# Kernel tuning notes

Measured on AMD Instinct MI355X. Metric: run time of the kernel, lower is better.

## Reference

```python
import jax, jax.numpy as jnp
import numpy as np

SIGMA = 4.0
RADIUS = int(4.0 * SIGMA + 0.5)  # scipy gaussian_filter truncate=4.0 -> radius 16


def _gaussian_kernel():
    x = jnp.arange(-RADIUS, RADIUS + 1, dtype=jnp.float32)
    k = jnp.exp(-0.5 * (x / SIGMA) ** 2)
    return k / k.sum()


def _blur_last_axis(x):
    # separable 1D gaussian along last axis with reflect padding (scipy default mode)
    k = _gaussian_kernel()
    pad = [(0, 0)] * (x.ndim - 1) + [(RADIUS, RADIUS)]
    xp = jnp.pad(x, pad, mode='reflect')
    xr = xp.reshape(-1, 1, xp.shape[-1])  # [N, C=1, L]
    out = jax.lax.conv_general_dilated(xr, k.reshape(1, 1, -1), (1,), 'VALID')
    return out.reshape(x.shape)


def _gaussian_blur2d(img):
    # img: [B, H, W]
    img = _blur_last_axis(img)                       # blur W
    img = jnp.swapaxes(_blur_last_axis(jnp.swapaxes(img, -1, -2)), -1, -2)  # blur H
    return img


def setup_inputs() -> dict:
    key = jax.random.key(0)
    k1, k2 = jax.random.split(key)
    M, Q, D = 50000, 3136, 1024
    return {
        'coreset': jax.random.normal(k1, (M, D), dtype=jnp.float32),
        'features': jax.random.normal(k2, (Q, D), dtype=jnp.float32),
        'batchsize': 4,
        'grid_h': 28,
        'grid_w': 28,
        'out_h': 224,
        'out_w': 224,
    }


def reference(coreset, features, batchsize, grid_h, grid_w, out_h, out_w):
    # _compute_batchwise_differences: sqrt(clamp(|a|^2 - 2ab + |b|^2, 0))
    a2 = jnp.sum(coreset * coreset, axis=-1, keepdims=True)      # [M, 1]
    b2 = jnp.sum(features * features, axis=-1)[None, :]           # [1, Q]
    ab = jnp.einsum('md,qd->mq', coreset, features)               # [M, Q]
    dists = jnp.sqrt(jnp.clip(a2 - 2.0 * ab + b2, 0.0, None))     # [M, Q]
    patch_scores = dists.min(axis=0)                              # [Q] = min(0).values

    # unpatch_scores + PatchMaker.score (max over patches)
    per_image = patch_scores.reshape(batchsize, -1)               # [B, P]
    image_scores = per_image.max(axis=-1)                         # [B]

    # RescaleSegmentor.convert_to_segmentation: bilinear upsample + gaussian blur
    grid = patch_scores.reshape(batchsize, grid_h, grid_w)        # [B, Hp, Wp]
    masks = jax.image.resize(grid, (batchsize, out_h, out_w), method='bilinear')
    masks = _gaussian_blur2d(masks)                               # sigma=4 smoothing
    return image_scores, masks
```

## Files before the change

kernel.cpp:

```cpp
#include <hip/hip_runtime.h>


typedef unsigned short ushort_t;
typedef unsigned int uint32;
typedef __bf16 bf16x8 __attribute__((ext_vector_type(8)));
typedef float f32x4 __attribute__((ext_vector_type(4)));

#define M_ROWS 50000
#define M_PAD  50176
#define M_TILES 196
#define Q_ROWS 3136
#define Q_PAD  3328
#define Q_TILES 13
#define DDIM   1024
#define NKT    16
#define FLT_BIG 3.402823466e+38f

typedef __attribute__((address_space(1))) const void* as1_cvoid;
typedef __attribute__((address_space(3))) void* as3_void;

__device__ __forceinline__ void load16_lds(const void* g, void* l) {
  __builtin_amdgcn_global_load_lds((as1_cvoid)g, (as3_void)l, 16, 0, 0);
}

__device__ __forceinline__ ushort_t f2bf(float f) {
  uint32 u = __float_as_uint(f);
  u += 0x7FFFu + ((u >> 16) & 1u);
  return (ushort_t)(u >> 16);
}
__device__ __forceinline__ uint32 f2key(float f) {
  uint32 b = __float_as_uint(f);
  return (b & 0x80000000u) ? ~b : (b | 0x80000000u);
}
__device__ __forceinline__ float key2f(uint32 k) {
  uint32 b = (k & 0x80000000u) ? (k ^ 0x80000000u) : ~k;
  return __uint_as_float(b);
}

#define WAITVM6 asm volatile("s_waitcnt vmcnt(6)" ::: "memory")
#define WAITVM0 asm volatile("s_waitcnt vmcnt(0)" ::: "memory")
#define WAITVM8 asm volatile("s_waitcnt vmcnt(8)" ::: "memory")
#define LGKM0   asm volatile("s_waitcnt lgkmcnt(0)" ::: "memory")
#define BAR()   __builtin_amdgcn_s_barrier()

__global__ void k_init(uint32* __restrict__ mk) {
  int i = blockIdx.x * 256 + threadIdx.x;
  if (i < Q_PAD) mk[i] = 0xFFFFFFFFu;
}

__global__ void k_convert(const float* __restrict__ src, ushort_t* __restrict__ dst,
                          float* __restrict__ norm, int valid_rows, float pad_norm) {
  const int row = blockIdx.x * 4 + (threadIdx.x >> 6);
  const int lane = threadIdx.x & 63;
  if (row < valid_rows) {
    const float4* s = (const float4*)(src + (size_t)row * DDIM);
    ushort4* d = (ushort4*)(dst + (size_t)row * DDIM);
    float ss = 0.f;
    #pragma unroll
    for (int u = 0; u < 4; ++u) {
      const float4 v = s[lane + 64 * u];
      ss += v.x * v.x + v.y * v.y + v.z * v.z + v.w * v.w;
      ushort4 o;
      o.x = f2bf(v.x); o.y = f2bf(v.y); o.z = f2bf(v.z); o.w = f2bf(v.w);
      d[lane + 64 * u] = o;
    }
    #pragma unroll
    for (int off = 32; off; off >>= 1) ss += __shfl_xor(ss, off);
    if (lane == 0) norm[row] = ss;
  } else {
    ushort4 z; z.x = z.y = z.z = z.w = 0;
    ushort4* d = (ushort4*)(dst + (size_t)row * DDIM);
    #pragma unroll
    for (int u = 0; u < 4; ++u) d[lane + 64 * u] = z;
    if (lane == 0) norm[row] = pad_norm;
  }
}

__global__ __launch_bounds__(512, 2) void k_gemm_min(
    const ushort_t* __restrict__ A,
    const ushort_t* __restrict__ B,
    const float* __restrict__ a2, const float* __restrict__ b2,
    uint32* __restrict__ mk) {
  __shared__ __align__(16) ushort_t As[2][256 * 64];
  __shared__ __align__(16) ushort_t Bs[2][256 * 64];
  __shared__ float a2s[256];
  __shared__ float red[4][64];

  const int tid = threadIdx.x;
  const int lane = tid & 63;
  const int wid = tid >> 6;
  const int wr = wid >> 2;
  const int wc = wid & 3;

  const int nwg = M_TILES * Q_TILES;
  const int q8 = nwg >> 3, r8 = nwg & 7;
  const int w = blockIdx.x;
  const int xcd = w & 7, idx = w >> 3;
  const int nw = (xcd < r8 ? xcd * (q8 + 1) : r8 * (q8 + 1) + (xcd - r8) * q8) + idx;
  const int mt = nw / Q_TILES;
  const int qt = nw - mt * Q_TILES;
  const int m0 = mt * 256;
  const int q0 = qt * 256;

  if (tid < 256) a2s[tid] = a2[m0 + tid];

  f32x4 acc[8][4];
  #pragma unroll
  for (int i = 0; i < 8; ++i)
    #pragma unroll
    for (int j = 0; j < 4; ++j)
      #pragma unroll
      for (int e = 0; e < 4; ++e) acc[i][j][e] = 0.f;

  const int kb = lane >> 4;
  const int col = lane & 15;
  const int swz = col & 7;

  const int swc = (tid & 7) ^ ((tid >> 3) & 7);
  const ushort_t* Abase = A + (size_t)(m0 + (tid >> 3)) * DDIM + swc * 8;
  const ushort_t* Bbase = B + (size_t)(q0 + (tid >> 3)) * DDIM + swc * 8;
  const int ldsoff = wid * 512;

  #define STG_A(bufi, row0, v) \
    load16_lds(Abase + (size_t)(row0) * DDIM + (v) * 64, &As[bufi][(row0) * 64] + ldsoff)
  #define STG_B(bufi, row0, v) \
    load16_lds(Bbase + (size_t)(row0) * DDIM + (v) * 64, &Bs[bufi][(row0) * 64] + ldsoff)

  #define LDA(row, kk) (*reinterpret_cast<const bf16x8*>( \
      &As[buf][(row) * 64 + ((((kk) * 4 + kb) ^ swz) << 3)]))
  #define LDB(row, kk) (*reinterpret_cast<const bf16x8*>( \
      &Bs[buf][(row) * 64 + ((((kk) * 4 + kb) ^ swz) << 3)]))

  STG_B(0, 0, 0);   STG_B(0, 64, 0);  STG_B(0, 128, 0); STG_B(0, 192, 0);
  STG_A(0, 0, 0);   STG_A(0, 128, 0); STG_A(0, 64, 0);  STG_A(0, 192, 0);
  STG_B(1, 0, 1);   STG_B(1, 64, 1);  STG_B(1, 128, 1); STG_B(1, 192, 1);
  STG_A(1, 0, 1);   STG_A(1, 128, 1); STG_A(1, 64, 1);  STG_A(1, 192, 1);
  WAITVM8;
  BAR();

  #define MFMA_ROW(q_)                                                        \
    _Pragma("unroll")                                                         \
    for (int m = 0; m < 2; ++m)                                               \
      _Pragma("unroll")                                                       \
      for (int n = 0; n < 4; ++n)                                             \
        _Pragma("unroll")                                                     \
        for (int kk = 0; kk < 2; ++kk)                                        \
          acc[(q_) * 2 + m][n] = __builtin_amdgcn_mfma_f32_16x16x32_bf16(     \
              af[m][kk], bff[n][kk], acc[(q_) * 2 + m][n], 0, 0, 0);

  #define KTILE(t, bufp_)                                                     \
  {                                                                           \
    const int buf = (bufp_);                                                  \
    bf16x8 bff[4][2], af[2][2];                                               \
                               \
    _Pragma("unroll")                                                         \
    for (int n = 0; n < 4; ++n)                                               \
      _Pragma("unroll")                                                       \
      for (int kk = 0; kk < 2; ++kk) bff[n][kk] = LDB(wc * 64 + n * 16 + col, kk); \
    _Pragma("unroll")                                                         \
    for (int m = 0; m < 2; ++m)                                               \
      _Pragma("unroll")                                                       \
      for (int kk = 0; kk < 2; ++kk) af[m][kk] = LDA(wr * 128 + m * 16 + col, kk); \
    if ((t) >= 1 && (t) <= NKT - 2) {                                         \
      STG_A(buf ^ 1, 64, (t) + 1); STG_A(buf ^ 1, 192, (t) + 1);              \
    }                                                                         \
    BAR(); LGKM0;                                                             \
    __builtin_amdgcn_s_setprio(1); MFMA_ROW(0); __builtin_amdgcn_s_setprio(0);\
    BAR();                                                                    \
                                       \
    _Pragma("unroll")                                                         \
    for (int m = 0; m < 2; ++m)                                               \
      _Pragma("unroll")                                                       \
      for (int kk = 0; kk < 2; ++kk)                                          \
        af[m][kk] = LDA(wr * 128 + 32 + m * 16 + col, kk);                    \
    if ((t) <= NKT - 3) { STG_B(buf, 0, (t) + 2); STG_B(buf, 64, (t) + 2); }  \
    BAR(); LGKM0;                                                             \
    __builtin_amdgcn_s_setprio(1); MFMA_ROW(1); __builtin_amdgcn_s_setprio(0);\
    BAR();                                                                    \
                                       \
    _Pragma("unroll")                                                         \
    for (int m = 0; m < 2; ++m)                                               \
      _Pragma("unroll")                                                       \
      for (int kk = 0; kk < 2; ++kk)                                          \
        af[m][kk] = LDA(wr * 128 + 64 + m * 16 + col, kk);                    \
    if ((t) <= NKT - 3) { STG_B(buf, 128, (t) + 2); STG_B(buf, 192, (t) + 2);}\
    BAR(); LGKM0;                                                             \
    __builtin_amdgcn_s_setprio(1); MFMA_ROW(2); __builtin_amdgcn_s_setprio(0);\
    BAR();                                                                    \
            \
    _Pragma("unroll")                                                         \
    for (int m = 0; m < 2; ++m)                                               \
      _Pragma("unroll")                                                       \
      for (int kk = 0; kk < 2; ++kk)                                          \
        af[m][kk] = LDA(wr * 128 + 96 + m * 16 + col, kk);                    \
    if ((t) <= NKT - 3) { STG_A(buf, 0, (t) + 2); STG_A(buf, 128, (t) + 2); } \
    BAR(); LGKM0;                                                             \
    __builtin_amdgcn_s_setprio(1); MFMA_ROW(3); __builtin_amdgcn_s_setprio(0);\
    if ((t) <= NKT - 3) { WAITVM6; }                                          \
    else if ((t) == NKT - 2) { WAITVM0; }                                     \
    BAR();                                                                    \
  }

  for (int tt = 0; tt < NKT / 2; ++tt) {
    const int te = 2 * tt;
    KTILE(te, 0)
    KTILE(te + 1, 1)
  }

  float v[4];
  #pragma unroll
  for (int j = 0; j < 4; ++j) {
    float mn = FLT_BIG;
    #pragma unroll
    for (int i = 0; i < 8; ++i)
      #pragma unroll
      for (int r = 0; r < 4; ++r) {
        const int ml = wr * 128 + i * 16 + kb * 4 + r;
        mn = fminf(mn, a2s[ml] - 2.0f * acc[i][j][r]);
      }
    mn = fminf(mn, __shfl_xor(mn, 16));
    mn = fminf(mn, __shfl_xor(mn, 32));
    v[j] = mn;
  }
  if (wr == 1 && lane < 16) {
    #pragma unroll
    for (int j = 0; j < 4; ++j) red[wc][j * 16 + lane] = v[j];
  }
  __syncthreads();
  if (wr == 0 && lane < 16) {
    #pragma unroll
    for (int j = 0; j < 4; ++j) {
      const int q = q0 + wc * 64 + j * 16 + lane;
      const float s = fminf(v[j], red[wc][j * 16 + lane]) + b2[q];
      atomicMin(&mk[q], f2key(s));
    }
  }
}

__global__ void k_finalize(const uint32* __restrict__ mk, float* __restrict__ ps,
                           float* __restrict__ out_scores) {
  const int b = blockIdx.x;
  const int tid = threadIdx.x;
  float vmax = -FLT_BIG;
  for (int t = tid; t < 784; t += 256) {
    const int q = b * 784 + t;
    float s = fmaxf(key2f(mk[q]), 0.f);
    const float p = sqrtf(s);
    ps[q] = p;
    vmax = fmaxf(vmax, p);
  }
  #pragma unroll
  for (int off = 32; off; off >>= 1) vmax = fmaxf(vmax, __shfl_xor(vmax, off));
  __shared__ float wm[4];
  if ((tid & 63) == 0) wm[tid >> 6] = vmax;
  __syncthreads();
  if (tid == 0) out_scores[b] = fmaxf(fmaxf(wm[0], wm[1]), fmaxf(wm[2], wm[3]));
}

__device__ __forceinline__ int reflect224(int i) {
  if (i < 0) i = -i;
  if (i > 223) i = 446 - i;
  return i;
}

__global__ void k_mkC(float* __restrict__ C) {
  const int idx = blockIdx.x * 256 + threadIdx.x;
  if (idx >= 224 * 28) return;
  const int o = idx / 28;
  const int g = idx - o * 28;
  float acc = 0.f, wsum = 0.f;
  for (int t = 0; t < 33; ++t) {
    const float d = (float)(t - 16);
    const float wb = expf(-0.03125f * d * d);
    wsum += wb;
    const int y = reflect224(o + t - 16);
    float fy = ((float)y + 0.5f) * 0.125f - 0.5f;
    int iy = (int)floorf(fy);
    float wy = fy - (float)iy;
    if (iy < 0)   { iy = 0;  wy = 0.f; }
    if (iy >= 27) { iy = 27; wy = 0.f; }
    const int iy1 = min(iy + 1, 27);
    float bw = 0.f;
    if (g == iy)  bw += 1.f - wy;
    if (g == iy1) bw += wy;
    acc += wb * bw;
  }
  C[idx] = acc / wsum;
}

__global__ void k_mask1(const float* __restrict__ ps, const float* __restrict__ C,
                        float* __restrict__ T) {
  const int idx = blockIdx.x * 256 + threadIdx.x;
  if (idx >= 4 * 28 * 224) return;
  const int X = idx % 224;
  const int gy = (idx / 224) % 28;
  const int b = idx / (224 * 28);
  const float* Crow = C + X * 28;
  const float* prow = ps + (b * 28 + gy) * 28;
  float s = 0.f;
  #pragma unroll
  for (int gx = 0; gx < 28; ++gx) s += Crow[gx] * prow[gx];
  T[idx] = s;
}

__global__ void k_mask2(const float* __restrict__ T, const float* __restrict__ C,
                        float* __restrict__ out) {
  const int idx = blockIdx.x * 256 + threadIdx.x;
  if (idx >= 4 * 224 * 224) return;
  const int X = idx % 224;
  const int Y = (idx / 224) % 224;
  const int b = idx / (224 * 224);
  const float* Crow = C + Y * 28;
  float s = 0.f;
  #pragma unroll
  for (int gy = 0; gy < 28; ++gy) s += Crow[gy] * T[(b * 28 + gy) * 224 + X];
  out[idx] = s;
}

extern "C" void kernel_launch(void* const* d_in, const int* in_sizes, int n_in,
                              void* d_out, int out_size, void* d_ws, size_t ws_size,
                              hipStream_t stream) {
  const float* cs = (const float*)d_in[0];
  const float* ft = (const float*)d_in[1];
  float* out = (float*)d_out;

  const size_t OFF_FT = (size_t)M_PAD * DDIM * 2;
  const size_t OFF_A2 = OFF_FT + (size_t)Q_PAD * DDIM * 2;
  const size_t OFF_B2 = OFF_A2 + (size_t)M_PAD * 4;
  const size_t OFF_MK = OFF_B2 + (size_t)Q_PAD * 4;
  const size_t OFF_PS = OFF_MK + (size_t)Q_PAD * 4;
  const size_t OFF_C  = OFF_PS + (size_t)Q_ROWS * 4;
  const size_t OFF_T  = OFF_C + (size_t)224 * 28 * 4;

  char* ws = (char*)d_ws;
  ushort_t* csb = (ushort_t*)(ws);
  ushort_t* ftb = (ushort_t*)(ws + OFF_FT);
  float* a2 = (float*)(ws + OFF_A2);
  float* b2 = (float*)(ws + OFF_B2);
  uint32* mk = (uint32*)(ws + OFF_MK);
  float* ps = (float*)(ws + OFF_PS);
  float* C  = (float*)(ws + OFF_C);
  float* T  = (float*)(ws + OFF_T);

  k_init<<<(Q_PAD + 255) / 256, 256, 0, stream>>>(mk);
  k_convert<<<M_PAD / 4, 256, 0, stream>>>(cs, csb, a2, M_ROWS, FLT_BIG);
  k_convert<<<Q_PAD / 4, 256, 0, stream>>>(ft, ftb, b2, Q_ROWS, 0.f);
  k_gemm_min<<<M_TILES * Q_TILES, 512, 0, stream>>>(csb, ftb, a2, b2, mk);
  k_finalize<<<4, 256, 0, stream>>>(mk, ps, out);
  k_mkC<<<(224 * 28 + 255) / 256, 256, 0, stream>>>(C);
  k_mask1<<<(4 * 28 * 224 + 255) / 256, 256, 0, stream>>>(ps, C, T);
  k_mask2<<<(4 * 224 * 224 + 255) / 256, 256, 0, stream>>>(T, C, out + 4);
}
```

Baseline: 649.7 us.

## Double-buffer A fragments and prefetch next tile's LDS reads during MFMAs

The GEMM main loop now keeps two sets of A fragment registers (afA/afB). The next quarter's A rows are read from LDS while the current quarter's MFMAs issue, and the explicit lgkmcnt(0) waits are removed. At the end of each k-tile, the next tile's B fragments and first A fragment are preloaded from the other LDS buffer during the last MFMA quarter. The goal is to hide LDS read latency behind MFMA work. In exchange, register pressure rises, and correctness now depends on the compiler-inserted waits and on the barrier ordering against the async global-to-LDS writes.

```diff
diff --git a/kernel.cpp b/kernel.cpp
--- a/kernel.cpp
+++ b/kernel.cpp
@@ -40,7 +40,6 @@
 #define WAITVM6 asm volatile("s_waitcnt vmcnt(6)" ::: "memory")
 #define WAITVM0 asm volatile("s_waitcnt vmcnt(0)" ::: "memory")
 #define WAITVM8 asm volatile("s_waitcnt vmcnt(8)" ::: "memory")
-#define LGKM0   asm volatile("s_waitcnt lgkmcnt(0)" ::: "memory")
 #define BAR()   __builtin_amdgcn_s_barrier()
 
 __global__ void k_init(uint32* __restrict__ mk) {
@@ -126,19 +125,29 @@
   #define STG_B(bufi, row0, v) \
     load16_lds(Bbase + (size_t)(row0) * DDIM + (v) * 64, &Bs[bufi][(row0) * 64] + ldsoff)
 
-  #define LDA(row, kk) (*reinterpret_cast<const bf16x8*>( \
-      &As[buf][(row) * 64 + ((((kk) * 4 + kb) ^ swz) << 3)]))
-  #define LDB(row, kk) (*reinterpret_cast<const bf16x8*>( \
-      &Bs[buf][(row) * 64 + ((((kk) * 4 + kb) ^ swz) << 3)]))
-
-  STG_B(0, 0, 0);   STG_B(0, 64, 0);  STG_B(0, 128, 0); STG_B(0, 192, 0);
-  STG_A(0, 0, 0);   STG_A(0, 128, 0); STG_A(0, 64, 0);  STG_A(0, 192, 0);
-  STG_B(1, 0, 1);   STG_B(1, 64, 1);  STG_B(1, 128, 1); STG_B(1, 192, 1);
-  STG_A(1, 0, 1);   STG_A(1, 128, 1); STG_A(1, 64, 1);  STG_A(1, 192, 1);
-  WAITVM8;
-  BAR();
-
-  #define MFMA_ROW(q_)                                                        \
+  #define LDAf(bi, row, kk) (*reinterpret_cast<const bf16x8*>( \
+      &As[bi][(row) * 64 + ((((kk) * 4 + kb) ^ swz) << 3)]))
+  #define LDBf(bi, row, kk) (*reinterpret_cast<const bf16x8*>( \
+      &Bs[bi][(row) * 64 + ((((kk) * 4 + kb) ^ swz) << 3)]))
+
+  bf16x8 bff[4][2];
+  bf16x8 afA[2][2], afB[2][2];
+
+  #define READ_BFF(bi)                                                        \
+    _Pragma("unroll")                                                         \
+    for (int n = 0; n < 4; ++n)                                               \
+      _Pragma("unroll")                                                       \
+      for (int kk = 0; kk < 2; ++kk)                                          \
+        bff[n][kk] = LDBf(bi, wc * 64 + n * 16 + col, kk);
+
+  #define READ_AF(dst_, bi, mbase_)                                           \
+    _Pragma("unroll")                                                         \
+    for (int m = 0; m < 2; ++m)                                               \
+      _Pragma("unroll")                                                       \
+      for (int kk = 0; kk < 2; ++kk)                                          \
+        dst_[m][kk] = LDAf(bi, wr * 128 + (mbase_) + m * 16 + col, kk);
+
+  #define MFMA_Q(q_, af_)                                                     \
     _Pragma("unroll")                                                         \
     for (int m = 0; m < 2; ++m)                                               \
       _Pragma("unroll")                                                       \
@@ -146,58 +155,62 @@
         _Pragma("unroll")                                                     \
         for (int kk = 0; kk < 2; ++kk)                                        \
           acc[(q_) * 2 + m][n] = __builtin_amdgcn_mfma_f32_16x16x32_bf16(     \
-              af[m][kk], bff[n][kk], acc[(q_) * 2 + m][n], 0, 0, 0);
+              af_[m][kk], bff[n][kk], acc[(q_) * 2 + m][n], 0, 0, 0);
+
+  STG_B(0, 0, 0);   STG_B(0, 64, 0);  STG_B(0, 128, 0); STG_B(0, 192, 0);
+  STG_A(0, 0, 0);   STG_A(0, 64, 0);  STG_A(0, 128, 0); STG_A(0, 192, 0);
+  STG_B(1, 0, 1);   STG_B(1, 64, 1);  STG_B(1, 128, 1); STG_B(1, 192, 1);
+  STG_A(1, 0, 1);   STG_A(1, 64, 1);  STG_A(1, 128, 1); STG_A(1, 192, 1);
+  WAITVM8;
+  BAR();
+  READ_BFF(0);
+  READ_AF(afA, 0, 0);
 
   #define KTILE(t, bufp_)                                                     \
   {                                                                           \
     const int buf = (bufp_);                                                  \
-    bf16x8 bff[4][2], af[2][2];                                               \
-                               \
-    _Pragma("unroll")                                                         \
-    for (int n = 0; n < 4; ++n)                                               \
-      _Pragma("unroll")                                                       \
-      for (int kk = 0; kk < 2; ++kk) bff[n][kk] = LDB(wc * 64 + n * 16 + col, kk); \
-    _Pragma("unroll")                                                         \
-    for (int m = 0; m < 2; ++m)                                               \
-      _Pragma("unroll")                                                       \
-      for (int kk = 0; kk < 2; ++kk) af[m][kk] = LDA(wr * 128 + m * 16 + col, kk); \
+                                                                      \
+    __builtin_amdgcn_s_setprio(1);                                            \
+    READ_AF(afB, buf, 32);                                                    \
+    MFMA_Q(0, afA);                                                           \
+    __builtin_amdgcn_s_setprio(0);                                            \
+    BAR();                                                                    \
+                                                                      \
     if ((t) >= 1 && (t) <= NKT - 2) {                                         \
       STG_A(buf ^ 1, 64, (t) + 1); STG_A(buf ^ 1, 192, (t) + 1);              \
     }                                                                         \
-    BAR(); LGKM0;                                                             \
-    __builtin_amdgcn_s_setprio(1); MFMA_ROW(0); __builtin_amdgcn_s_setprio(0);\
-    BAR();                                                                    \
-                                       \
-    _Pragma("unroll")                                                         \
-    for (int m = 0; m < 2; ++m)                                               \
-      _Pragma("unroll")                                                       \
-      for (int kk = 0; kk < 2; ++kk)                                          \
-        af[m][kk] = LDA(wr * 128 + 32 + m * 16 + col, kk);                    \
+    BAR();                                                                    \
+                                                                      \
+    __builtin_amdgcn_s_setprio(1);                                            \
+    READ_AF(afA, buf, 64);                                                    \
+    MFMA_Q(1, afB);                                                           \
+    __builtin_amdgcn_s_setprio(0);                                            \
+    BAR();                                                                    \
+                                                                      \
     if ((t) <= NKT - 3) { STG_B(buf, 0, (t) + 2); STG_B(buf, 64, (t) + 2); }  \
-    BAR(); LGKM0;                                                             \
-    __builtin_amdgcn_s_setprio(1); MFMA_ROW(1); __builtin_amdgcn_s_setprio(0);\
-    BAR();                                                                    \
-                                       \
-    _Pragma("unroll")                                                         \
-    for (int m = 0; m < 2; ++m)                                               \
-      _Pragma("unroll")                                                       \
-      for (int kk = 0; kk < 2; ++kk)                                          \
-        af[m][kk] = LDA(wr * 128 + 64 + m * 16 + col, kk);                    \
+    BAR();                                                                    \
+                                                                      \
+    __builtin_amdgcn_s_setprio(1);                                            \
+    READ_AF(afB, buf, 96);                                                    \
+    MFMA_Q(2, afA);                                                           \
+    __builtin_amdgcn_s_setprio(0);                                            \
+    BAR();                                                                    \
+                                                                      \
     if ((t) <= NKT - 3) { STG_B(buf, 128, (t) + 2); STG_B(buf, 192, (t) + 2);}\
-    BAR(); LGKM0;                                                             \
-    __builtin_amdgcn_s_setprio(1); MFMA_ROW(2); __builtin_amdgcn_s_setprio(0);\
-    BAR();                                                                    \
-            \
-    _Pragma("unroll")                                                         \
-    for (int m = 0; m < 2; ++m)                                               \
-      _Pragma("unroll")                                                       \
-      for (int kk = 0; kk < 2; ++kk)                                          \
-        af[m][kk] = LDA(wr * 128 + 96 + m * 16 + col, kk);                    \
-    if ((t) <= NKT - 3) { STG_A(buf, 0, (t) + 2); STG_A(buf, 128, (t) + 2); } \
-    BAR(); LGKM0;                                                             \
-    __builtin_amdgcn_s_setprio(1); MFMA_ROW(3); __builtin_amdgcn_s_setprio(0);\
-    if ((t) <= NKT - 3) { WAITVM6; }                                          \
-    else if ((t) == NKT - 2) { WAITVM0; }                                     \
+    BAR();                                                                    \
+                              \
+    if ((t) <= NKT - 3) {                                                     \
+      STG_A(buf, 0, (t) + 2); STG_A(buf, 128, (t) + 2);                       \
+      WAITVM6;                                                                \
+    } else if ((t) == NKT - 2) {                                              \
+      WAITVM0;                                                                \
+    }                                                                         \
+    BAR();                                                                    \
+             \
+    __builtin_amdgcn_s_setprio(1);                                            \
+    MFMA_Q(3, afB);                                                           \
+    if ((t) <= NKT - 2) { READ_BFF(buf ^ 1); READ_AF(afA, buf ^ 1, 0); }      \
+    __builtin_amdgcn_s_setprio(0);                                            \
     BAR();                                                                    \
   }
 
```

New measurement: 636.3 us. -2.1%, faster.
